# Optimization experiments

Hardware: AMD Instinct MI355X
Metric: run time of the kernel (lower is better)

## Reference

```python
import jax, jax.numpy as jnp
import numpy as np

N_NODES = 100000
N_EDGES = 1600000
IN_C = 128
HID_C = 32
HEADS = 4
OUT_C = 40
N_GRAPHS = 64
NEG_SLOPE = 0.2  # PyG GATConv default


def setup_inputs() -> dict:
    key = jax.random.key(0)
    ks = jax.random.split(key, 12)
    x = jax.random.normal(ks[0], (N_NODES, IN_C), dtype=jnp.float32)
    edge_index = jax.random.randint(ks[1], (2, N_EDGES), 0, N_NODES, dtype=jnp.int64)
    batch = jnp.sort(jax.random.randint(ks[2], (N_NODES,), 0, N_GRAPHS, dtype=jnp.int64))
    s1 = 1.0 / np.sqrt(IN_C)
    s2 = 1.0 / np.sqrt(HEADS * HID_C)
    W1 = jax.random.normal(ks[3], (IN_C, HEADS * HID_C), dtype=jnp.float32) * s1
    a1_src = jax.random.normal(ks[4], (HEADS, HID_C), dtype=jnp.float32) * s1
    a1_dst = jax.random.normal(ks[5], (HEADS, HID_C), dtype=jnp.float32) * s1
    b1 = jnp.zeros((HEADS * HID_C,), dtype=jnp.float32)
    W2 = jax.random.normal(ks[6], (HEADS * HID_C, OUT_C), dtype=jnp.float32) * s2
    a2_src = jax.random.normal(ks[7], (1, OUT_C), dtype=jnp.float32) * s2
    a2_dst = jax.random.normal(ks[8], (1, OUT_C), dtype=jnp.float32) * s2
    b2 = jnp.zeros((OUT_C,), dtype=jnp.float32)
    return {"x": x, "edge_index": edge_index, "batch": batch,
            "W1": W1, "a1_src": a1_src, "a1_dst": a1_dst, "b1": b1,
            "W2": W2, "a2_src": a2_src, "a2_dst": a2_dst, "b2": b2}


def gat_conv(x, src, dst, W, a_src, a_dst, bias, heads, out_c, concat):
    """PyG-style GATConv (eval mode, self-loops included in src/dst)."""
    N = x.shape[0]
    h = (x @ W).reshape(N, heads, out_c)              # [N,H,C]
    alpha_s = jnp.einsum('nhc,hc->nh', h, a_src)      # [N,H]
    alpha_d = jnp.einsum('nhc,hc->nh', h, a_dst)
    e = alpha_s[src] + alpha_d[dst]                   # [E,H]
    e = jnp.where(e > 0, e, NEG_SLOPE * e)            # LeakyReLU(0.2)
    # segment softmax over edges grouped by destination node
    m = jax.ops.segment_max(e, dst, num_segments=N)   # [N,H]
    ex = jnp.exp(e - m[dst])
    denom = jax.ops.segment_sum(ex, dst, num_segments=N)
    alpha = ex / (denom[dst] + 1e-16)                 # [E,H]
    msg = h[src] * alpha[..., None]                   # [E,H,C]
    out = jax.ops.segment_sum(msg, dst, num_segments=N)  # [N,H,C]
    if concat:
        out = out.reshape(N, heads * out_c)
    else:
        out = out.mean(axis=1)
    return out + bias


def reference(x, edge_index, batch, W1, a1_src, a1_dst, b1, W2, a2_src, a2_dst, b2):
    N = x.shape[0]
    # add self-loops (PyG GATConv default add_self_loops=True)
    loop = jnp.arange(N, dtype=edge_index.dtype)
    src = jnp.concatenate([edge_index[0], loop])
    dst = jnp.concatenate([edge_index[1], loop])
    h = gat_conv(x, src, dst, W1, a1_src, a1_dst, b1, HEADS, HID_C, concat=True)
    h = jax.nn.elu(h)
    h = gat_conv(h, src, dst, W2, a2_src, a2_dst, b2, 1, OUT_C, concat=False)
    # global mean pool over graphs
    sums = jax.ops.segment_sum(h, batch, num_segments=N_GRAPHS)
    counts = jax.ops.segment_sum(jnp.ones((N,), dtype=h.dtype), batch, num_segments=N_GRAPHS)
    return sums / jnp.maximum(counts, 1.0)[:, None]
```

## Files before the change

### kernel.cpp

```cpp
#include <hip/hip_runtime.h>

#define NNODES 100000
#define NEDGES 1600000
#define ETOT   1700000
#define NGRAPH 64
#define NEG    0.2f
#define NB_SCAN 98
#define NPART  8
#define DPP    12500
#define SCAT_BPP 128
#define SCAT_CH  ((ETOT + SCAT_BPP - 1) / SCAT_BPP)
#define PCH    1024

using f32x2 = __attribute__((ext_vector_type(2))) float;

__device__ __forceinline__ float f4get(const float4& v, int j) {
    return j == 0 ? v.x : j == 1 ? v.y : j == 2 ? v.z : v.w;
}

__device__ __forceinline__ unsigned short f2bf(float f) {
    unsigned u = __float_as_uint(f);
    u = (u + 0x7fffu + ((u >> 16) & 1u)) >> 16;
    return (unsigned short)u;
}
__device__ __forceinline__ float bf_lo(unsigned u) { return __uint_as_float(u << 16); }
__device__ __forceinline__ float bf_hi(unsigned u) { return __uint_as_float(u & 0xffff0000u); }

__global__ __launch_bounds__(256) void k_hist(const int* __restrict__ ei,
                                              int* __restrict__ cnt,
                                              int* __restrict__ rank) {
    int base = blockIdx.x * 1024 + threadIdx.x;
    int e0 = base, e1 = base + 256, e2 = base + 512, e3 = base + 768;
    int d0 = 0, d1 = 0, d2 = 0, d3 = 0;
    bool v0 = e0 < ETOT, v1 = e1 < ETOT, v2 = e2 < ETOT, v3 = e3 < ETOT;
    if (v0) d0 = (e0 < NEDGES) ? ei[NEDGES + e0] : e0 - NEDGES;
    if (v1) d1 = (e1 < NEDGES) ? ei[NEDGES + e1] : e1 - NEDGES;
    if (v2) d2 = (e2 < NEDGES) ? ei[NEDGES + e2] : e2 - NEDGES;
    if (v3) d3 = (e3 < NEDGES) ? ei[NEDGES + e3] : e3 - NEDGES;
    int r0 = 0, r1 = 0, r2 = 0, r3 = 0;
    if (v0) r0 = atomicAdd(&cnt[d0], 1);
    if (v1) r1 = atomicAdd(&cnt[d1], 1);
    if (v2) r2 = atomicAdd(&cnt[d2], 1);
    if (v3) r3 = atomicAdd(&cnt[d3], 1);
    if (v0) rank[e0] = r0;
    if (v1) rank[e1] = r1;
    if (v2) rank[e2] = r2;
    if (v3) rank[e3] = r3;
}

__global__ __launch_bounds__(256) void k_scan1(const int* __restrict__ cnt,
                                               int* __restrict__ excl,
                                               int* __restrict__ bsum) {
    __shared__ int tmp[256];
    int t = threadIdx.x;
    int base = blockIdx.x * 1024 + t * 4;
    int v0 = base + 0 < NNODES ? cnt[base + 0] : 0;
    int v1 = base + 1 < NNODES ? cnt[base + 1] : 0;
    int v2 = base + 2 < NNODES ? cnt[base + 2] : 0;
    int v3 = base + 3 < NNODES ? cnt[base + 3] : 0;
    int tot = v0 + v1 + v2 + v3;
    tmp[t] = tot;
    __syncthreads();
    for (int off = 1; off < 256; off <<= 1) {
        int x = (t >= off) ? tmp[t - off] : 0;
        __syncthreads();
        tmp[t] += x;
        __syncthreads();
    }
    int tbase = tmp[t] - tot;
    if (base + 0 < NNODES) excl[base + 0] = tbase;
    if (base + 1 < NNODES) excl[base + 1] = tbase + v0;
    if (base + 2 < NNODES) excl[base + 2] = tbase + v0 + v1;
    if (base + 3 < NNODES) excl[base + 3] = tbase + v0 + v1 + v2;
    if (t == 255) bsum[blockIdx.x] = tmp[255];
}

__global__ __launch_bounds__(256) void k_offs(const int* __restrict__ excl,
                                              const int* __restrict__ bsum,
                                              int* __restrict__ offs) {
    __shared__ int sp;
    int b = blockIdx.x, t = threadIdx.x;
    if (t == 0) {
        int p = 0;
        for (int i = 0; i < b; ++i) p += bsum[i];
        sp = p;
    }
    __syncthreads();
    int prefix = sp;
#pragma unroll
    for (int j = 0; j < 4; ++j) {
        int idx = b * 1024 + t * 4 + j;
        if (idx < NNODES) offs[idx] = excl[idx] + prefix;
    }
}

__global__ __launch_bounds__(256) void k_scatter(const int* __restrict__ ei,
                                                 const int* __restrict__ rank,
                                                 const int* __restrict__ offs,
                                                 int* __restrict__ csr_src) {
    int p = blockIdx.x & (NPART - 1);
    int chunk = blockIdx.x / NPART;
    int dlo = p * DPP, dhi = dlo + DPP;
    int e0 = chunk * SCAT_CH;
    int e1 = e0 + SCAT_CH; if (e1 > ETOT) e1 = ETOT;
    for (int e = e0 + threadIdx.x; e < e1; e += 256) {
        int d = (e < NEDGES) ? ei[NEDGES + e] : e - NEDGES;
        if (d >= dlo && d < dhi) {
            int s = (e < NEDGES) ? ei[e] : d;
            csr_src[offs[d] + rank[e]] = s;
        }
    }
}

__global__ __launch_bounds__(256, 4) void k_gemm1(const float* __restrict__ x,
                                               const float* __restrict__ W1,
                                               const float* __restrict__ a1s,
                                               const float* __restrict__ a1d,
                                               unsigned* __restrict__ h1q,
                                               float* __restrict__ as1,
                                               float* __restrict__ ad1) {
    __shared__ float sX[64 * 128];
    int t = threadIdx.x;
    int nbase = blockIdx.x * 64;
    int nrows = NNODES - nbase; if (nrows > 64) nrows = 64;
    {
        const float4* X4 = (const float4*)(x + (size_t)nbase * 128);
        float4* sX4 = (float4*)sX;
        for (int i = t; i < nrows * 32; i += 256) sX4[i] = X4[i];
    }
    __syncthreads();

    int colg = t & 31, rowg = t >> 5;
    int c0 = colg * 4, n0 = rowg * 8;
    float acc[8][4];
#pragma unroll
    for (int i = 0; i < 8; ++i)
        acc[i][0] = acc[i][1] = acc[i][2] = acc[i][3] = 0.f;

    for (int k = 0; k < 128; k += 4) {
        float4 w0 = *(const float4*)&W1[(size_t)(k + 0) * 128 + c0];
        float4 w1 = *(const float4*)&W1[(size_t)(k + 1) * 128 + c0];
        float4 w2 = *(const float4*)&W1[(size_t)(k + 2) * 128 + c0];
        float4 w3 = *(const float4*)&W1[(size_t)(k + 3) * 128 + c0];
#pragma unroll
        for (int i = 0; i < 8; ++i) {
            float4 xv = *(const float4*)&sX[(n0 + i) * 128 + k];
            acc[i][0] = fmaf(xv.x, w0.x, acc[i][0]); acc[i][1] = fmaf(xv.x, w0.y, acc[i][1]);
            acc[i][2] = fmaf(xv.x, w0.z, acc[i][2]); acc[i][3] = fmaf(xv.x, w0.w, acc[i][3]);
            acc[i][0] = fmaf(xv.y, w1.x, acc[i][0]); acc[i][1] = fmaf(xv.y, w1.y, acc[i][1]);
            acc[i][2] = fmaf(xv.y, w1.z, acc[i][2]); acc[i][3] = fmaf(xv.y, w1.w, acc[i][3]);
            acc[i][0] = fmaf(xv.z, w2.x, acc[i][0]); acc[i][1] = fmaf(xv.z, w2.y, acc[i][1]);
            acc[i][2] = fmaf(xv.z, w2.z, acc[i][2]); acc[i][3] = fmaf(xv.z, w2.w, acc[i][3]);
            acc[i][0] = fmaf(xv.w, w3.x, acc[i][0]); acc[i][1] = fmaf(xv.w, w3.y, acc[i][1]);
            acc[i][2] = fmaf(xv.w, w3.z, acc[i][2]); acc[i][3] = fmaf(xv.w, w3.w, acc[i][3]);
        }
    }

    int head = colg >> 3;
    float ws0 = a1s[c0], ws1 = a1s[c0 + 1], ws2 = a1s[c0 + 2], ws3 = a1s[c0 + 3];
    float wd0 = a1d[c0], wd1 = a1d[c0 + 1], wd2 = a1d[c0 + 2], wd3 = a1d[c0 + 3];
#pragma unroll
    for (int i = 0; i < 8; ++i) {
        int n = n0 + i;
        float ps = acc[i][0] * ws0 + acc[i][1] * ws1 + acc[i][2] * ws2 + acc[i][3] * ws3;
        float pd = acc[i][0] * wd0 + acc[i][1] * wd1 + acc[i][2] * wd2 + acc[i][3] * wd3;
        ps += __shfl_xor(ps, 1); ps += __shfl_xor(ps, 2); ps += __shfl_xor(ps, 4);
        pd += __shfl_xor(pd, 1); pd += __shfl_xor(pd, 2); pd += __shfl_xor(pd, 4);
        if (n < nrows) {
            int q = __builtin_amdgcn_cvt_pk_fp8_f32(acc[i][0], acc[i][1], 0, false);
            q = __builtin_amdgcn_cvt_pk_fp8_f32(acc[i][2], acc[i][3], q, true);
            h1q[((size_t)(nbase + n)) * 32 + colg] = (unsigned)q;
            if ((colg & 7) == 0) {
                as1[(size_t)(nbase + n) * 4 + head] = ps;
                ad1[(size_t)(nbase + n) * 4 + head] = pd;
            }
        }
    }
}

__global__ __launch_bounds__(256) void k_node1(const int* __restrict__ csr_src,
        const int* __restrict__ offs, const int* __restrict__ cnt,
        const unsigned* __restrict__ h1q,
        const float4* __restrict__ as1v, const float4* __restrict__ ad1v,
        unsigned* __restrict__ out1b) {
    __shared__ float4 exbuf[8][32];
    int t = threadIdx.x;
    int grp = t >> 5, lane = t & 31;
    int node = blockIdx.x * 8 + grp;
    if (node >= NNODES) return;
    int head = lane >> 3;
    int off = offs[node];
    int deg = cnt[node];
    float4 adv = ad1v[node];
    float4 dp = make_float4(0.f, 0.f, 0.f, 0.f);
    float4 acc = make_float4(0.f, 0.f, 0.f, 0.f);
    const float* exs = (const float*)&exbuf[grp][0];

    for (int base = 0; base < deg; base += 32) {
        int m = deg - base; if (m > 32) m = 32;
        int sv = 0;
        if (lane < m) {
            sv = csr_src[off + base + lane];
            float4 av = as1v[sv];
            float v; float4 e;
            v = av.x + adv.x; v = v > 0.f ? v : NEG * v; e.x = __expf(v);
            v = av.y + adv.y; v = v > 0.f ? v : NEG * v; e.y = __expf(v);
            v = av.z + adv.z; v = v > 0.f ? v : NEG * v; e.z = __expf(v);
            v = av.w + adv.w; v = v > 0.f ? v : NEG * v; e.w = __expf(v);
            exbuf[grp][lane] = e;
            dp.x += e.x; dp.y += e.y; dp.z += e.z; dp.w += e.w;
        }
        __builtin_amdgcn_wave_barrier();
        int i = 0;
        for (; i + 4 <= m; i += 4) {
            int s0 = __shfl(sv, i + 0, 32);
            int s1 = __shfl(sv, i + 1, 32);
            int s2 = __shfl(sv, i + 2, 32);
            int s3 = __shfl(sv, i + 3, 32);
            unsigned q0 = h1q[(size_t)s0 * 32 + lane];
            unsigned q1 = h1q[(size_t)s1 * 32 + lane];
            unsigned q2 = h1q[(size_t)s2 * 32 + lane];
            unsigned q3 = h1q[(size_t)s3 * 32 + lane];
            float a0 = exs[(i + 0) * 4 + head];
            float a1 = exs[(i + 1) * 4 + head];
            float a2 = exs[(i + 2) * 4 + head];
            float a3 = exs[(i + 3) * 4 + head];
            f32x2 lo, hi;
            lo = __builtin_amdgcn_cvt_pk_f32_fp8((int)q0, false);
            hi = __builtin_amdgcn_cvt_pk_f32_fp8((int)q0, true);
            acc.x = fmaf(lo.x, a0, acc.x); acc.y = fmaf(lo.y, a0, acc.y);
            acc.z = fmaf(hi.x, a0, acc.z); acc.w = fmaf(hi.y, a0, acc.w);
            lo = __builtin_amdgcn_cvt_pk_f32_fp8((int)q1, false);
            hi = __builtin_amdgcn_cvt_pk_f32_fp8((int)q1, true);
            acc.x = fmaf(lo.x, a1, acc.x); acc.y = fmaf(lo.y, a1, acc.y);
            acc.z = fmaf(hi.x, a1, acc.z); acc.w = fmaf(hi.y, a1, acc.w);
            lo = __builtin_amdgcn_cvt_pk_f32_fp8((int)q2, false);
            hi = __builtin_amdgcn_cvt_pk_f32_fp8((int)q2, true);
            acc.x = fmaf(lo.x, a2, acc.x); acc.y = fmaf(lo.y, a2, acc.y);
            acc.z = fmaf(hi.x, a2, acc.z); acc.w = fmaf(hi.y, a2, acc.w);
            lo = __builtin_amdgcn_cvt_pk_f32_fp8((int)q3, false);
            hi = __builtin_amdgcn_cvt_pk_f32_fp8((int)q3, true);
            acc.x = fmaf(lo.x, a3, acc.x); acc.y = fmaf(lo.y, a3, acc.y);
            acc.z = fmaf(hi.x, a3, acc.z); acc.w = fmaf(hi.y, a3, acc.w);
        }
        for (; i < m; ++i) {
            int s = __shfl(sv, i, 32);
            float a = exs[i * 4 + head];
            unsigned hq = h1q[(size_t)s * 32 + lane];
            f32x2 lo = __builtin_amdgcn_cvt_pk_f32_fp8((int)hq, false);
            f32x2 hi = __builtin_amdgcn_cvt_pk_f32_fp8((int)hq, true);
            acc.x = fmaf(lo.x, a, acc.x);
            acc.y = fmaf(lo.y, a, acc.y);
            acc.z = fmaf(hi.x, a, acc.z);
            acc.w = fmaf(hi.y, a, acc.w);
        }
        __builtin_amdgcn_wave_barrier();
    }
#pragma unroll
    for (int msk = 1; msk < 32; msk <<= 1) {
        dp.x += __shfl_xor(dp.x, msk, 32);
        dp.y += __shfl_xor(dp.y, msk, 32);
        dp.z += __shfl_xor(dp.z, msk, 32);
        dp.w += __shfl_xor(dp.w, msk, 32);
    }
    float inv = 1.f / f4get(dp, head);
    unsigned p0 = (unsigned)f2bf(acc.x * inv) | ((unsigned)f2bf(acc.y * inv) << 16);
    unsigned p1 = (unsigned)f2bf(acc.z * inv) | ((unsigned)f2bf(acc.w * inv) << 16);
    uint2 pk; pk.x = p0; pk.y = p1;
    *(uint2*)&out1b[(size_t)node * 64 + lane * 2] = pk;
}

__global__ __launch_bounds__(256) void k_gemm2(const unsigned* __restrict__ in_b,
                                               const float* __restrict__ W2,
                                               const float* __restrict__ b1,
                                               const float* __restrict__ a2s,
                                               const float* __restrict__ a2d,
                                               unsigned short* __restrict__ h2b,
                                               float* __restrict__ as2,
                                               float* __restrict__ ad2) {
    __shared__ float sW[128 * 40];
    __shared__ float sX[128 * 132];
    int t = threadIdx.x;
    for (int i = t; i < 128 * 40 / 4; i += 256) ((float4*)sW)[i] = ((const float4*)W2)[i];
    int nbase = blockIdx.x * 128;
    int nrows = NNODES - nbase; if (nrows > 128) nrows = 128;
    {
        const uint4* X4 = (const uint4*)(in_b + (size_t)nbase * 64);
        for (int i = t; i < nrows * 16; i += 256) {
            int row = i >> 4, c8 = i & 15;
            uint4 v = X4[i];
            float4 bb0 = *(const float4*)&b1[c8 * 8];
            float4 bb1 = *(const float4*)&b1[c8 * 8 + 4];
            float f0 = bf_lo(v.x) + bb0.x, f1 = bf_hi(v.x) + bb0.y;
            float f2 = bf_lo(v.y) + bb0.z, f3 = bf_hi(v.y) + bb0.w;
            float f4 = bf_lo(v.z) + bb1.x, f5 = bf_hi(v.z) + bb1.y;
            float f6 = bf_lo(v.w) + bb1.z, f7 = bf_hi(v.w) + bb1.w;
            f0 = f0 > 0.f ? f0 : __expf(f0) - 1.f;
            f1 = f1 > 0.f ? f1 : __expf(f1) - 1.f;
            f2 = f2 > 0.f ? f2 : __expf(f2) - 1.f;
            f3 = f3 > 0.f ? f3 : __expf(f3) - 1.f;
            f4 = f4 > 0.f ? f4 : __expf(f4) - 1.f;
            f5 = f5 > 0.f ? f5 : __expf(f5) - 1.f;
            f6 = f6 > 0.f ? f6 : __expf(f6) - 1.f;
            f7 = f7 > 0.f ? f7 : __expf(f7) - 1.f;
            float* sp = &sX[row * 132 + c8 * 8];
            *(float4*)sp       = make_float4(f0, f1, f2, f3);
            *(float4*)(sp + 4) = make_float4(f4, f5, f6, f7);
        }
    }
    __syncthreads();

    int colg = t & 7, nodeg = t >> 3;
    int c0 = colg * 5;
    float acc[4][5];
#pragma unroll
    for (int i = 0; i < 4; ++i)
#pragma unroll
        for (int c = 0; c < 5; ++c) acc[i][c] = 0.f;

    for (int k = 0; k < 128; k += 4) {
        float4 xv[4];
#pragma unroll
        for (int i = 0; i < 4; ++i)
            xv[i] = *(const float4*)&sX[(nodeg + 32 * i) * 132 + k];
#pragma unroll
        for (int j = 0; j < 4; ++j) {
            float w0 = sW[(k + j) * 40 + c0 + 0];
            float w1 = sW[(k + j) * 40 + c0 + 1];
            float w2 = sW[(k + j) * 40 + c0 + 2];
            float w3 = sW[(k + j) * 40 + c0 + 3];
            float w4 = sW[(k + j) * 40 + c0 + 4];
#pragma unroll
            for (int i = 0; i < 4; ++i) {
                float xs = f4get(xv[i], j);
                acc[i][0] = fmaf(xs, w0, acc[i][0]);
                acc[i][1] = fmaf(xs, w1, acc[i][1]);
                acc[i][2] = fmaf(xs, w2, acc[i][2]);
                acc[i][3] = fmaf(xs, w3, acc[i][3]);
                acc[i][4] = fmaf(xs, w4, acc[i][4]);
            }
        }
    }

    float ws0 = a2s[c0], ws1 = a2s[c0 + 1], ws2 = a2s[c0 + 2], ws3 = a2s[c0 + 3], ws4 = a2s[c0 + 4];
    float wd0 = a2d[c0], wd1 = a2d[c0 + 1], wd2 = a2d[c0 + 2], wd3 = a2d[c0 + 3], wd4 = a2d[c0 + 4];
#pragma unroll
    for (int i = 0; i < 4; ++i) {
        int n = nodeg + 32 * i;
        float ps = acc[i][0]*ws0 + acc[i][1]*ws1 + acc[i][2]*ws2 + acc[i][3]*ws3 + acc[i][4]*ws4;
        float pd = acc[i][0]*wd0 + acc[i][1]*wd1 + acc[i][2]*wd2 + acc[i][3]*wd3 + acc[i][4]*wd4;
        ps += __shfl_xor(ps, 1); ps += __shfl_xor(ps, 2); ps += __shfl_xor(ps, 4);
        pd += __shfl_xor(pd, 1); pd += __shfl_xor(pd, 2); pd += __shfl_xor(pd, 4);
        if (n < nrows) {
            unsigned short* hp = h2b + (size_t)(nbase + n) * 40 + c0;
#pragma unroll
            for (int c = 0; c < 5; ++c) hp[c] = f2bf(acc[i][c]);
            if (colg == 0) {
                as2[nbase + n] = ps;
                ad2[nbase + n] = pd;
            }
        }
    }
}

__global__ __launch_bounds__(256) void k_node2(const int* __restrict__ csr_src,
        const int* __restrict__ offs, const int* __restrict__ cnt,
        const unsigned short* __restrict__ h2b,
        const float* __restrict__ as2, const float* __restrict__ ad2,
        float* __restrict__ out2) {
    int t = threadIdx.x;
    int grp = t >> 4, lane = t & 15;
    int node = blockIdx.x * 16 + grp;
    if (node >= NNODES) return;
    int off = offs[node];
    int deg = cnt[node];
    float adv = ad2[node];
    float dp = 0.f;
    float4 acc = make_float4(0.f, 0.f, 0.f, 0.f);

    for (int base = 0; base < deg; base += 16) {
        int m = deg - base; if (m > 16) m = 16;
        int sv = 0; float ex = 0.f;
        if (lane < m) {
            sv = csr_src[off + base + lane];
            float v = as2[sv] + adv;
            v = v > 0.f ? v : NEG * v;
            ex = __expf(v);
            dp += ex;
        }
        int i = 0;
        for (; i + 4 <= m; i += 4) {
            int s0 = __shfl(sv, i + 0, 16);
            int s1 = __shfl(sv, i + 1, 16);
            int s2 = __shfl(sv, i + 2, 16);
            int s3 = __shfl(sv, i + 3, 16);
            float a0 = __shfl(ex, i + 0, 16);
            float a1 = __shfl(ex, i + 1, 16);
            float a2 = __shfl(ex, i + 2, 16);
            float a3 = __shfl(ex, i + 3, 16);
            if (lane < 10) {
                uint2 h0 = *(const uint2*)(h2b + (size_t)s0 * 40 + lane * 4);
                uint2 h1 = *(const uint2*)(h2b + (size_t)s1 * 40 + lane * 4);
                uint2 h2 = *(const uint2*)(h2b + (size_t)s2 * 40 + lane * 4);
                uint2 h3 = *(const uint2*)(h2b + (size_t)s3 * 40 + lane * 4);
                acc.x = fmaf(bf_lo(h0.x), a0, acc.x); acc.y = fmaf(bf_hi(h0.x), a0, acc.y);
                acc.z = fmaf(bf_lo(h0.y), a0, acc.z); acc.w = fmaf(bf_hi(h0.y), a0, acc.w);
                acc.x = fmaf(bf_lo(h1.x), a1, acc.x); acc.y = fmaf(bf_hi(h1.x), a1, acc.y);
                acc.z = fmaf(bf_lo(h1.y), a1, acc.z); acc.w = fmaf(bf_hi(h1.y), a1, acc.w);
                acc.x = fmaf(bf_lo(h2.x), a2, acc.x); acc.y = fmaf(bf_hi(h2.x), a2, acc.y);
                acc.z = fmaf(bf_lo(h2.y), a2, acc.z); acc.w = fmaf(bf_hi(h2.y), a2, acc.w);
                acc.x = fmaf(bf_lo(h3.x), a3, acc.x); acc.y = fmaf(bf_hi(h3.x), a3, acc.y);
                acc.z = fmaf(bf_lo(h3.y), a3, acc.z); acc.w = fmaf(bf_hi(h3.y), a3, acc.w);
            }
        }
        for (; i < m; ++i) {
            int s = __shfl(sv, i, 16);
            float a = __shfl(ex, i, 16);
            if (lane < 10) {
                uint2 hv = *(const uint2*)(h2b + (size_t)s * 40 + lane * 4);
                acc.x = fmaf(bf_lo(hv.x), a, acc.x);
                acc.y = fmaf(bf_hi(hv.x), a, acc.y);
                acc.z = fmaf(bf_lo(hv.y), a, acc.z);
                acc.w = fmaf(bf_hi(hv.y), a, acc.w);
            }
        }
    }
#pragma unroll
    for (int msk = 1; msk < 16; msk <<= 1) dp += __shfl_xor(dp, msk, 16);
    float inv = 1.f / dp;
    if (lane < 10) {
        float4 o; o.x = acc.x * inv; o.y = acc.y * inv; o.z = acc.z * inv; o.w = acc.w * inv;
        *(float4*)(out2 + (size_t)node * 40 + lane * 4) = o;
    }
}

__global__ __launch_bounds__(256) void k_pool1(const float* __restrict__ out2,
        const int* __restrict__ batch, float* __restrict__ partial) {
    int t = threadIdx.x;
    if (t >= 240) return;
    int r = t / 40, c = t - r * 40;
    int base = blockIdx.x * PCH;
    int end = base + PCH; if (end > NNODES) end = NNODES;
    float sum = 0.f; int gcur = -1;
    for (int n = base + r; n < end; n += 6) {
        int g = batch[n];
        if (g != gcur) {
            if (gcur >= 0) unsafeAtomicAdd(&partial[gcur * 40 + c], sum);
            gcur = g; sum = 0.f;
        }
        sum += out2[(size_t)n * 40 + c];
    }
    if (gcur >= 0) unsafeAtomicAdd(&partial[gcur * 40 + c], sum);
}

__global__ void k_pool2(const float* __restrict__ partial, const int* __restrict__ batch,
                        const float* __restrict__ b2, float* __restrict__ out) {
    int i = blockIdx.x * 256 + threadIdx.x;
    if (i >= NGRAPH * 40) return;
    int g = i / 40, c = i - g * 40;
    int lo, hi;
    { int a = 0, b = NNODES; while (a < b) { int m = (a + b) >> 1; if (batch[m] < g) a = m + 1; else b = m; } lo = a; }
    { int a = lo, b = NNODES; while (a < b) { int m = (a + b) >> 1; if (batch[m] < g + 1) a = m + 1; else b = m; } hi = a; }
    int cntg = hi - lo;
    out[i] = cntg > 0 ? partial[i] / (float)cntg + b2[c] : 0.f;
}

extern "C" void kernel_launch(void* const* d_in, const int* in_sizes, int n_in,
                              void* d_out, int out_size, void* d_ws, size_t ws_size,
                              hipStream_t stream) {
    const float* x    = (const float*)d_in[0];
    const int*   ei   = (const int*)d_in[1];
    const int*   batch= (const int*)d_in[2];
    const float* W1   = (const float*)d_in[3];
    const float* a1s  = (const float*)d_in[4];
    const float* a1d  = (const float*)d_in[5];
    const float* b1   = (const float*)d_in[6];
    const float* W2   = (const float*)d_in[7];
    const float* a2s  = (const float*)d_in[8];
    const float* a2d  = (const float*)d_in[9];
    const float* b2   = (const float*)d_in[10];
    float* out = (float*)d_out;

    int* cnt      = (int*)d_ws;
    float* partial= (float*)(cnt + NNODES);
    int* excl     = (int*)(partial + NGRAPH * 40);
    int* offs     = excl + NNODES;
    int* bsum     = offs + NNODES;
    int* rank     = bsum + 128;
    int* csr      = rank + ETOT;
    float* as1    = (float*)(csr + ETOT);
    float* ad1    = as1 + (size_t)NNODES * 4;
    unsigned* h1q = (unsigned*)(ad1 + (size_t)NNODES * 4);
    unsigned* out1b = h1q + (size_t)NNODES * 32;
    float* as2    = (float*)(out1b + (size_t)NNODES * 64);
    float* ad2    = as2 + NNODES;
    unsigned short* h2b = (unsigned short*)(ad2 + NNODES);
    float* out2   = (float*)(h2b + (size_t)NNODES * 40);

    hipMemsetAsync(d_ws, 0, ((size_t)NNODES + NGRAPH * 40) * sizeof(int), stream);

    k_hist<<<(ETOT + 1023) / 1024, 256, 0, stream>>>(ei, cnt, rank);
    k_scan1<<<NB_SCAN, 256, 0, stream>>>(cnt, excl, bsum);
    k_offs<<<NB_SCAN, 256, 0, stream>>>(excl, bsum, offs);
    k_scatter<<<NPART * SCAT_BPP, 256, 0, stream>>>(ei, rank, offs, csr);

    k_gemm1<<<(NNODES + 63) / 64, 256, 0, stream>>>(x, W1, a1s, a1d, h1q, as1, ad1);
    k_node1<<<(NNODES + 7) / 8, 256, 0, stream>>>(csr, offs, cnt, h1q,
                                                  (const float4*)as1, (const float4*)ad1, out1b);

    k_gemm2<<<(NNODES + 127) / 128, 256, 0, stream>>>(out1b, W2, b1, a2s, a2d, h2b, as2, ad2);
    k_node2<<<(NNODES + 15) / 16, 256, 0, stream>>>(csr, offs, cnt, h2b, as2, ad2, out2);

    k_pool1<<<(NNODES + PCH - 1) / PCH, 256, 0, stream>>>(out2, batch, partial);
    k_pool2<<<(NGRAPH * 40 + 255) / 256, 256, 0, stream>>>(partial, batch, b2, out);
}
```

Baseline: 387.3 us.

## Fuse histogram and first GEMM into one launch; unroll scatter loop

Merges the degree histogram and the layer-1 projection GEMM into a single kernel, with odd blocks doing the histogram and even blocks doing the GEMM, so the two independent phases run concurrently and one launch is removed. It also unrolls the scatter loop four-way so more index loads are in flight per iteration. The fused kernel declares the 32 KB shared buffer for every block, which may reduce occupancy for the histogram blocks, and idle even blocks past the GEMM range simply exit.

New measurement: 342.3 us. 11.6% less time.

```diff
diff --git a/kernel.cpp b/kernel.cpp
--- a/kernel.cpp
+++ b/kernel.cpp
@@ -11,6 +11,8 @@
 #define SCAT_BPP 128
 #define SCAT_CH  ((ETOT + SCAT_BPP - 1) / SCAT_BPP)
 #define PCH    1024
+#define NHB    1661
+#define NGB    1563
 
 using f32x2 = __attribute__((ext_vector_type(2))) float;
 
@@ -26,26 +28,92 @@
 __device__ __forceinline__ float bf_lo(unsigned u) { return __uint_as_float(u << 16); }
 __device__ __forceinline__ float bf_hi(unsigned u) { return __uint_as_float(u & 0xffff0000u); }
 
-__global__ __launch_bounds__(256) void k_hist(const int* __restrict__ ei,
-                                              int* __restrict__ cnt,
-                                              int* __restrict__ rank) {
-    int base = blockIdx.x * 1024 + threadIdx.x;
-    int e0 = base, e1 = base + 256, e2 = base + 512, e3 = base + 768;
-    int d0 = 0, d1 = 0, d2 = 0, d3 = 0;
-    bool v0 = e0 < ETOT, v1 = e1 < ETOT, v2 = e2 < ETOT, v3 = e3 < ETOT;
-    if (v0) d0 = (e0 < NEDGES) ? ei[NEDGES + e0] : e0 - NEDGES;
-    if (v1) d1 = (e1 < NEDGES) ? ei[NEDGES + e1] : e1 - NEDGES;
-    if (v2) d2 = (e2 < NEDGES) ? ei[NEDGES + e2] : e2 - NEDGES;
-    if (v3) d3 = (e3 < NEDGES) ? ei[NEDGES + e3] : e3 - NEDGES;
-    int r0 = 0, r1 = 0, r2 = 0, r3 = 0;
-    if (v0) r0 = atomicAdd(&cnt[d0], 1);
-    if (v1) r1 = atomicAdd(&cnt[d1], 1);
-    if (v2) r2 = atomicAdd(&cnt[d2], 1);
-    if (v3) r3 = atomicAdd(&cnt[d3], 1);
-    if (v0) rank[e0] = r0;
-    if (v1) rank[e1] = r1;
-    if (v2) rank[e2] = r2;
-    if (v3) rank[e3] = r3;
+__global__ __launch_bounds__(256, 4) void k_fused1(const int* __restrict__ ei,
+        int* __restrict__ cnt, int* __restrict__ rank,
+        const float* __restrict__ x, const float* __restrict__ W1,
+        const float* __restrict__ a1s, const float* __restrict__ a1d,
+        unsigned* __restrict__ h1q, float* __restrict__ as1, float* __restrict__ ad1) {
+    __shared__ float sX[64 * 128];
+    int bid = blockIdx.x;
+    if (bid & 1) {
+        int hb = bid >> 1;
+        int base = hb * 1024 + threadIdx.x;
+        int e0 = base, e1 = base + 256, e2 = base + 512, e3 = base + 768;
+        bool v0 = e0 < ETOT, v1 = e1 < ETOT, v2 = e2 < ETOT, v3 = e3 < ETOT;
+        int d0 = 0, d1 = 0, d2 = 0, d3 = 0;
+        if (v0) d0 = (e0 < NEDGES) ? ei[NEDGES + e0] : e0 - NEDGES;
+        if (v1) d1 = (e1 < NEDGES) ? ei[NEDGES + e1] : e1 - NEDGES;
+        if (v2) d2 = (e2 < NEDGES) ? ei[NEDGES + e2] : e2 - NEDGES;
+        if (v3) d3 = (e3 < NEDGES) ? ei[NEDGES + e3] : e3 - NEDGES;
+        int r0 = 0, r1 = 0, r2 = 0, r3 = 0;
+        if (v0) r0 = atomicAdd(&cnt[d0], 1);
+        if (v1) r1 = atomicAdd(&cnt[d1], 1);
+        if (v2) r2 = atomicAdd(&cnt[d2], 1);
+        if (v3) r3 = atomicAdd(&cnt[d3], 1);
+        if (v0) rank[e0] = r0;
+        if (v1) rank[e1] = r1;
+        if (v2) rank[e2] = r2;
+        if (v3) rank[e3] = r3;
+        return;
+    }
+    int gb = bid >> 1;
+    if (gb >= NGB) return;
+    int t = threadIdx.x;
+    int nbase = gb * 64;
+    int nrows = NNODES - nbase; if (nrows > 64) nrows = 64;
+    {
+        const float4* X4 = (const float4*)(x + (size_t)nbase * 128);
+        float4* sX4 = (float4*)sX;
+        for (int i = t; i < nrows * 32; i += 256) sX4[i] = X4[i];
+    }
+    __syncthreads();
+
+    int colg = t & 31, rowg = t >> 5;
+    int c0 = colg * 4, n0 = rowg * 8;
+    float acc[8][4];
+#pragma unroll
+    for (int i = 0; i < 8; ++i)
+        acc[i][0] = acc[i][1] = acc[i][2] = acc[i][3] = 0.f;
+
+    for (int k = 0; k < 128; k += 4) {
+        float4 w0 = *(const float4*)&W1[(size_t)(k + 0) * 128 + c0];
+        float4 w1 = *(const float4*)&W1[(size_t)(k + 1) * 128 + c0];
+        float4 w2 = *(const float4*)&W1[(size_t)(k + 2) * 128 + c0];
+        float4 w3 = *(const float4*)&W1[(size_t)(k + 3) * 128 + c0];
+#pragma unroll
+        for (int i = 0; i < 8; ++i) {
+            float4 xv = *(const float4*)&sX[(n0 + i) * 128 + k];
+            acc[i][0] = fmaf(xv.x, w0.x, acc[i][0]); acc[i][1] = fmaf(xv.x, w0.y, acc[i][1]);
+            acc[i][2] = fmaf(xv.x, w0.z, acc[i][2]); acc[i][3] = fmaf(xv.x, w0.w, acc[i][3]);
+            acc[i][0] = fmaf(xv.y, w1.x, acc[i][0]); acc[i][1] = fmaf(xv.y, w1.y, acc[i][1]);
+            acc[i][2] = fmaf(xv.y, w1.z, acc[i][2]); acc[i][3] = fmaf(xv.y, w1.w, acc[i][3]);
+            acc[i][0] = fmaf(xv.z, w2.x, acc[i][0]); acc[i][1] = fmaf(xv.z, w2.y, acc[i][1]);
+            acc[i][2] = fmaf(xv.z, w2.z, acc[i][2]); acc[i][3] = fmaf(xv.z, w2.w, acc[i][3]);
+            acc[i][0] = fmaf(xv.w, w3.x, acc[i][0]); acc[i][1] = fmaf(xv.w, w3.y, acc[i][1]);
+            acc[i][2] = fmaf(xv.w, w3.z, acc[i][2]); acc[i][3] = fmaf(xv.w, w3.w, acc[i][3]);
+        }
+    }
+
+    int head = colg >> 3;
+    float ws0 = a1s[c0], ws1 = a1s[c0 + 1], ws2 = a1s[c0 + 2], ws3 = a1s[c0 + 3];
+    float wd0 = a1d[c0], wd1 = a1d[c0 + 1], wd2 = a1d[c0 + 2], wd3 = a1d[c0 + 3];
+#pragma unroll
+    for (int i = 0; i < 8; ++i) {
+        int n = n0 + i;
+        float ps = acc[i][0] * ws0 + acc[i][1] * ws1 + acc[i][2] * ws2 + acc[i][3] * ws3;
+        float pd = acc[i][0] * wd0 + acc[i][1] * wd1 + acc[i][2] * wd2 + acc[i][3] * wd3;
+        ps += __shfl_xor(ps, 1); ps += __shfl_xor(ps, 2); ps += __shfl_xor(ps, 4);
+        pd += __shfl_xor(pd, 1); pd += __shfl_xor(pd, 2); pd += __shfl_xor(pd, 4);
+        if (n < nrows) {
+            int q = __builtin_amdgcn_cvt_pk_fp8_f32(acc[i][0], acc[i][1], 0, false);
+            q = __builtin_amdgcn_cvt_pk_fp8_f32(acc[i][2], acc[i][3], q, true);
+            h1q[((size_t)(nbase + n)) * 32 + colg] = (unsigned)q;
+            if ((colg & 7) == 0) {
+                as1[(size_t)(nbase + n) * 4 + head] = ps;
+                ad1[(size_t)(nbase + n) * 4 + head] = pd;
+            }
+        }
+    }
 }
 
 __global__ __launch_bounds__(256) void k_scan1(const int* __restrict__ cnt,
@@ -103,77 +171,29 @@
     int dlo = p * DPP, dhi = dlo + DPP;
     int e0 = chunk * SCAT_CH;
     int e1 = e0 + SCAT_CH; if (e1 > ETOT) e1 = ETOT;
-    for (int e = e0 + threadIdx.x; e < e1; e += 256) {
-        int d = (e < NEDGES) ? ei[NEDGES + e] : e - NEDGES;
-        if (d >= dlo && d < dhi) {
-            int s = (e < NEDGES) ? ei[e] : d;
-            csr_src[offs[d] + rank[e]] = s;
-        }
-    }
-}
-
-__global__ __launch_bounds__(256, 4) void k_gemm1(const float* __restrict__ x,
-                                               const float* __restrict__ W1,
-                                               const float* __restrict__ a1s,
-                                               const float* __restrict__ a1d,
-                                               unsigned* __restrict__ h1q,
-                                               float* __restrict__ as1,
-                                               float* __restrict__ ad1) {
-    __shared__ float sX[64 * 128];
-    int t = threadIdx.x;
-    int nbase = blockIdx.x * 64;
-    int nrows = NNODES - nbase; if (nrows > 64) nrows = 64;
-    {
-        const float4* X4 = (const float4*)(x + (size_t)nbase * 128);
-        float4* sX4 = (float4*)sX;
-        for (int i = t; i < nrows * 32; i += 256) sX4[i] = X4[i];
-    }
-    __syncthreads();
-
-    int colg = t & 31, rowg = t >> 5;
-    int c0 = colg * 4, n0 = rowg * 8;
-    float acc[8][4];
-#pragma unroll
-    for (int i = 0; i < 8; ++i)
-        acc[i][0] = acc[i][1] = acc[i][2] = acc[i][3] = 0.f;
-
-    for (int k = 0; k < 128; k += 4) {
-        float4 w0 = *(const float4*)&W1[(size_t)(k + 0) * 128 + c0];
-        float4 w1 = *(const float4*)&W1[(size_t)(k + 1) * 128 + c0];
-        float4 w2 = *(const float4*)&W1[(size_t)(k + 2) * 128 + c0];
-        float4 w3 = *(const float4*)&W1[(size_t)(k + 3) * 128 + c0];
-#pragma unroll
-        for (int i = 0; i < 8; ++i) {
-            float4 xv = *(const float4*)&sX[(n0 + i) * 128 + k];
-            acc[i][0] = fmaf(xv.x, w0.x, acc[i][0]); acc[i][1] = fmaf(xv.x, w0.y, acc[i][1]);
-            acc[i][2] = fmaf(xv.x, w0.z, acc[i][2]); acc[i][3] = fmaf(xv.x, w0.w, acc[i][3]);
-            acc[i][0] = fmaf(xv.y, w1.x, acc[i][0]); acc[i][1] = fmaf(xv.y, w1.y, acc[i][1]);
-            acc[i][2] = fmaf(xv.y, w1.z, acc[i][2]); acc[i][3] = fmaf(xv.y, w1.w, acc[i][3]);
-            acc[i][0] = fmaf(xv.z, w2.x, acc[i][0]); acc[i][1] = fmaf(xv.z, w2.y, acc[i][1]);
-            acc[i][2] = fmaf(xv.z, w2.z, acc[i][2]); acc[i][3] = fmaf(xv.z, w2.w, acc[i][3]);
-            acc[i][0] = fmaf(xv.w, w3.x, acc[i][0]); acc[i][1] = fmaf(xv.w, w3.y, acc[i][1]);
-            acc[i][2] = fmaf(xv.w, w3.z, acc[i][2]); acc[i][3] = fmaf(xv.w, w3.w, acc[i][3]);
-        }
-    }
-
-    int head = colg >> 3;
-    float ws0 = a1s[c0], ws1 = a1s[c0 + 1], ws2 = a1s[c0 + 2], ws3 = a1s[c0 + 3];
-    float wd0 = a1d[c0], wd1 = a1d[c0 + 1], wd2 = a1d[c0 + 2], wd3 = a1d[c0 + 3];
-#pragma unroll
-    for (int i = 0; i < 8; ++i) {
-        int n = n0 + i;
-        float ps = acc[i][0] * ws0 + acc[i][1] * ws1 + acc[i][2] * ws2 + acc[i][3] * ws3;
-        float pd = acc[i][0] * wd0 + acc[i][1] * wd1 + acc[i][2] * wd2 + acc[i][3] * wd3;
-        ps += __shfl_xor(ps, 1); ps += __shfl_xor(ps, 2); ps += __shfl_xor(ps, 4);
-        pd += __shfl_xor(pd, 1); pd += __shfl_xor(pd, 2); pd += __shfl_xor(pd, 4);
-        if (n < nrows) {
-            int q = __builtin_amdgcn_cvt_pk_fp8_f32(acc[i][0], acc[i][1], 0, false);
-            q = __builtin_amdgcn_cvt_pk_fp8_f32(acc[i][2], acc[i][3], q, true);
-            h1q[((size_t)(nbase + n)) * 32 + colg] = (unsigned)q;
-            if ((colg & 7) == 0) {
-                as1[(size_t)(nbase + n) * 4 + head] = ps;
-                ad1[(size_t)(nbase + n) * 4 + head] = pd;
-            }
+    for (int e = e0 + threadIdx.x; e < e1; e += 1024) {
+        int eA = e, eB = e + 256, eC = e + 512, eD = e + 768;
+        bool vA = eA < e1, vB = eB < e1, vC = eC < e1, vD = eD < e1;
+        int dA = -1, dB = -1, dC = -1, dD = -1;
+        if (vA) dA = (eA < NEDGES) ? ei[NEDGES + eA] : eA - NEDGES;
+        if (vB) dB = (eB < NEDGES) ? ei[NEDGES + eB] : eB - NEDGES;
+        if (vC) dC = (eC < NEDGES) ? ei[NEDGES + eC] : eC - NEDGES;
+        if (vD) dD = (eD < NEDGES) ? ei[NEDGES + eD] : eD - NEDGES;
+        if (dA >= dlo && dA < dhi) {
+            int s = (eA < NEDGES) ? ei[eA] : dA;
+            csr_src[offs[dA] + rank[eA]] = s;
+        }
+        if (dB >= dlo && dB < dhi) {
+            int s = (eB < NEDGES) ? ei[eB] : dB;
+            csr_src[offs[dB] + rank[eB]] = s;
+        }
+        if (dC >= dlo && dC < dhi) {
+            int s = (eC < NEDGES) ? ei[eC] : dC;
+            csr_src[offs[dC] + rank[eC]] = s;
+        }
+        if (dD >= dlo && dD < dhi) {
+            int s = (eD < NEDGES) ? ei[eD] : dD;
+            csr_src[offs[dD] + rank[eD]] = s;
         }
     }
 }
@@ -499,12 +519,12 @@
 
     hipMemsetAsync(d_ws, 0, ((size_t)NNODES + NGRAPH * 40) * sizeof(int), stream);
 
-    k_hist<<<(ETOT + 1023) / 1024, 256, 0, stream>>>(ei, cnt, rank);
+    k_fused1<<<2 * NHB, 256, 0, stream>>>(ei, cnt, rank, x, W1, a1s, a1d, h1q, as1, ad1);
+
     k_scan1<<<NB_SCAN, 256, 0, stream>>>(cnt, excl, bsum);
     k_offs<<<NB_SCAN, 256, 0, stream>>>(excl, bsum, offs);
     k_scatter<<<NPART * SCAT_BPP, 256, 0, stream>>>(ei, rank, offs, csr);
 
-    k_gemm1<<<(NNODES + 63) / 64, 256, 0, stream>>>(x, W1, a1s, a1d, h1q, as1, ad1);
     k_node1<<<(NNODES + 7) / 8, 256, 0, stream>>>(csr, offs, cnt, h1q,
                                                   (const float4*)as1, (const float4*)ad1, out1b);
 
```
